# Performance work log

Hardware: AMD Instinct MI355X
Metric: run time of the kernel (lower is better)

## Reference

```python
import jax, jax.numpy as jnp
import numpy as np

B, L, C, H = 4, 2048, 512, 8
CH = C // H
EPS = 1e-5


def setup_inputs() -> dict:
    key = jax.random.key(0)
    k1, k2, k3 = jax.random.split(key, 3)
    return {
        "input_x": jax.random.normal(k1, (B, L, C), dtype=jnp.float32),
        "gamma": jnp.ones((C,), dtype=jnp.float32),
        "beta": jnp.zeros((C,), dtype=jnp.float32),
        "w_xyz": jax.random.normal(k2, (C, 3 * C), dtype=jnp.float32) * 0.02,
        "b_xyz": jnp.zeros((3 * C,), dtype=jnp.float32),
        "w_end": jax.random.normal(k3, (C, C), dtype=jnp.float32) * 0.02,
        "b_end": jnp.zeros((C,), dtype=jnp.float32),
    }


def reference(input_x, gamma, beta, w_xyz, b_xyz, w_end, b_end):
    b, l, c = input_x.shape
    h = H
    ch = c // h
    scale = 1.0 / np.sqrt(ch).astype(np.float32)

    # LayerNorm
    mu = jnp.mean(input_x, axis=-1, keepdims=True)
    var = jnp.var(input_x, axis=-1, keepdims=True)
    xn = (input_x - mu) / jnp.sqrt(var + EPS) * gamma + beta

    # xyz projection -> (3, b, h, l, ch)
    xyz = (xn @ w_xyz + b_xyz).reshape(b, l, 3, h, ch).transpose(2, 0, 3, 1, 4)
    q, k, v = xyz[0], xyz[1], xyz[2]

    # dot-product relevancy with sqr scale
    scores = jnp.einsum("bhqc,bhkc->bhqk", q * scale, k)
    attn = jax.nn.softmax(scores, axis=-1)

    # weighted sum -> (b, l, c)
    z = jnp.einsum("bhqk,bhkc->bhqc", attn, v).transpose(0, 2, 1, 3).reshape(b, l, c)
    z = z @ w_end + b_end
    return input_x + z
```

## Files before the change

### kernel.cpp

```cpp
#include <hip/hip_runtime.h>
#include <hip/hip_bf16.h>
#include <math.h>

constexpr int Bv = 4, Lv = 2048, Cv = 512, Hv = 8, CHv = 64;
constexpr int Mv = Bv * Lv;
constexpr int N3 = 3 * Cv;
constexpr float EPSv = 1e-5f;
constexpr float SCALEv = 0.125f;
constexpr float K2v = 0.125f * 1.44269504089f;
constexpr int LDST = 76;
constexpr int PSTR = 68;

typedef __attribute__((ext_vector_type(4))) float f32x4;
typedef __attribute__((ext_vector_type(8))) short bf16x8;

__device__ inline unsigned short f2bf(float f) {
  unsigned int u = __float_as_uint(f);
  unsigned int r = (u + 0x7fffu + ((u >> 16) & 1u)) >> 16;
  return (unsigned short)r;
}

__device__ __forceinline__ void async_copy16(void* lp, const void* gp) {
  __builtin_amdgcn_global_load_lds(
      (const __attribute__((address_space(1))) void*)gp,
      (__attribute__((address_space(3))) void*)lp, 16, 0, 0);
}

__global__ __launch_bounds__(256) void ln_kernel(const float* __restrict__ x,
                                                 const float* __restrict__ gamma,
                                                 const float* __restrict__ beta,
                                                 unsigned short* __restrict__ xnb) {
  const int row = blockIdx.x * 4 + (threadIdx.x >> 6);
  const int lane = threadIdx.x & 63;
  const float4* xr = reinterpret_cast<const float4*>(x + (size_t)row * Cv);
  float4 v0 = xr[lane];
  float4 v1 = xr[lane + 64];
  float s = v0.x + v0.y + v0.z + v0.w + v1.x + v1.y + v1.z + v1.w;
  float q = v0.x * v0.x + v0.y * v0.y + v0.z * v0.z + v0.w * v0.w +
            v1.x * v1.x + v1.y * v1.y + v1.z * v1.z + v1.w * v1.w;
#pragma unroll
  for (int m = 1; m < 64; m <<= 1) {
    s += __shfl_xor(s, m, 64);
    q += __shfl_xor(q, m, 64);
  }
  const float mu = s * (1.0f / Cv);
  const float var = q * (1.0f / Cv) - mu * mu;
  const float rstd = rsqrtf(var + EPSv);
  const float4* g4 = reinterpret_cast<const float4*>(gamma);
  const float4* b4 = reinterpret_cast<const float4*>(beta);
  float4 ga = g4[lane], gb = g4[lane + 64];
  float4 ba = b4[lane], bb = b4[lane + 64];
  ushort4 u0, u1;
  u0.x = f2bf((v0.x - mu) * rstd * ga.x + ba.x);
  u0.y = f2bf((v0.y - mu) * rstd * ga.y + ba.y);
  u0.z = f2bf((v0.z - mu) * rstd * ga.z + ba.z);
  u0.w = f2bf((v0.w - mu) * rstd * ga.w + ba.w);
  u1.x = f2bf((v1.x - mu) * rstd * gb.x + bb.x);
  u1.y = f2bf((v1.y - mu) * rstd * gb.y + bb.y);
  u1.z = f2bf((v1.z - mu) * rstd * gb.z + bb.z);
  u1.w = f2bf((v1.w - mu) * rstd * gb.w + bb.w);
  ushort4* xo = reinterpret_cast<ushort4*>(xnb + (size_t)row * Cv);
  xo[lane] = u0;
  xo[lane + 64] = u1;
}

__global__ __launch_bounds__(256) void transpose_f2b(const float* __restrict__ in,
                                                     unsigned short* __restrict__ out,
                                                     int R, int Cn) {
  __shared__ float Tl[64][65];
  const int t = threadIdx.x;
  const int tr = t >> 6, tc = t & 63;
  const int r0 = blockIdx.y * 64, c0 = blockIdx.x * 64;
#pragma unroll
  for (int i = 0; i < 16; ++i)
    Tl[tr + i * 4][tc] = in[(size_t)(r0 + tr + i * 4) * Cn + c0 + tc];
  __syncthreads();
#pragma unroll
  for (int i = 0; i < 16; ++i)
    out[(size_t)(c0 + tr + i * 4) * R + r0 + tc] = f2bf(Tl[tc][tr + i * 4]);
}

template <bool RES, bool OUTBF>
__global__ __launch_bounds__(256) void gemm_mfma(const unsigned short* __restrict__ A,
                                                 const unsigned short* __restrict__ Bt,
                                                 const float* __restrict__ bias,
                                                 const float* __restrict__ res,
                                                 float* __restrict__ Cf,
                                                 unsigned short* __restrict__ Cb,
                                                 int M, int N, int K) {
  __shared__ unsigned short Al[128 * 64];
  __shared__ unsigned short Bl[128 * 64];
  const int t = threadIdx.x;
  const int l = t & 63, w = t >> 6;
  const int lm = l & 15, lq = l >> 4;
  const int m0 = blockIdx.y * 128, n0 = blockIdx.x * 128;
  const int rw0 = (w >> 1) * 64, cw0 = (w & 1) * 64;

  f32x4 acc[4][4];
#pragma unroll
  for (int mi = 0; mi < 4; ++mi)
#pragma unroll
    for (int ni = 0; ni < 4; ++ni) acc[mi][ni] = f32x4{0.f, 0.f, 0.f, 0.f};

  const int sr8 = l >> 3;
  const int sc = l & 7;

  for (int k0 = 0; k0 < K; k0 += 64) {
#pragma unroll
    for (int j = 0; j < 4; ++j) {
      const int row = w * 32 + j * 8 + sr8;
      const int cs = sc ^ (row & 7);
      async_copy16(&Al[(w * 32 + j * 8) * 64],
                   A + (size_t)(m0 + row) * K + k0 + cs * 8);
      async_copy16(&Bl[(w * 32 + j * 8) * 64],
                   Bt + (size_t)(n0 + row) * K + k0 + cs * 8);
    }
    __syncthreads();

    bf16x8 af[4][2], bfr[4][2];
#pragma unroll
    for (int mi = 0; mi < 4; ++mi) {
      const int r = rw0 + mi * 16 + lm;
#pragma unroll
      for (int ks = 0; ks < 2; ++ks) {
        const int c = (ks * 4 + lq) ^ (r & 7);
        af[mi][ks] = *reinterpret_cast<const bf16x8*>(&Al[r * 64 + c * 8]);
      }
    }
#pragma unroll
    for (int ni = 0; ni < 4; ++ni) {
      const int r = cw0 + ni * 16 + lm;
#pragma unroll
      for (int ks = 0; ks < 2; ++ks) {
        const int c = (ks * 4 + lq) ^ (r & 7);
        bfr[ni][ks] = *reinterpret_cast<const bf16x8*>(&Bl[r * 64 + c * 8]);
      }
    }
#pragma unroll
    for (int ks = 0; ks < 2; ++ks)
#pragma unroll
      for (int mi = 0; mi < 4; ++mi)
#pragma unroll
        for (int ni = 0; ni < 4; ++ni)
          acc[mi][ni] = __builtin_amdgcn_mfma_f32_16x16x32_bf16(
              af[mi][ks], bfr[ni][ks], acc[mi][ni], 0, 0, 0);
    __syncthreads();
  }

#pragma unroll
  for (int mi = 0; mi < 4; ++mi)
#pragma unroll
    for (int ni = 0; ni < 4; ++ni) {
      const int col = n0 + cw0 + ni * 16 + lm;
      const float bv = bias[col];
#pragma unroll
      for (int r = 0; r < 4; ++r) {
        const int row = m0 + rw0 + mi * 16 + lq * 4 + r;
        float v = acc[mi][ni][r] + bv;
        if (RES) v += res[(size_t)row * N + col];
        if (OUTBF)
          Cb[(size_t)row * N + col] = f2bf(v);
        else
          Cf[(size_t)row * N + col] = v;
      }
    }
}

__global__ __launch_bounds__(256) void attn_mfma(const unsigned short* __restrict__ qkv,
                                                 unsigned short* __restrict__ zb) {
  __shared__ unsigned short Ks[64 * LDST];
  __shared__ unsigned short Vt[64 * LDST];
  __shared__ unsigned short Ps[64 * PSTR];

  const int t = threadIdx.x;
  const int l = t & 63, w = t >> 6;
  const int lm = l & 15, lq = l >> 4;

  const int f = blockIdx.x + 32 * blockIdx.y + 256 * blockIdx.z;
  const int n = (f & 7) * 128 + (f >> 3);
  const int qt = n & 31, h = (n >> 5) & 7, b = n >> 8;
  const int q0 = qt * 64;

  const unsigned short* base = qkv + (size_t)b * Lv * N3;
  const int kcol = Cv + h * CHv, vcol = 2 * Cv + h * CHv;

  bf16x8 qf0, qf1;
  {
    const unsigned short* qp = base + (size_t)(q0 + w * 16 + lm) * N3 + h * CHv + lq * 8;
    qf0 = *reinterpret_cast<const bf16x8*>(qp);
    qf1 = *reinterpret_cast<const bf16x8*>(qp + 32);
  }

  const int sr = t >> 3, sc = t & 7;

  bf16x8 kr0, kr1, vr0, vr1;
  {
    const unsigned short* kp = base + (size_t)sr * N3 + kcol + sc * 8;
    const unsigned short* vp = base + (size_t)sr * N3 + vcol + sc * 8;
    kr0 = *reinterpret_cast<const bf16x8*>(kp);
    kr1 = *reinterpret_cast<const bf16x8*>(kp + (size_t)32 * N3);
    vr0 = *reinterpret_cast<const bf16x8*>(vp);
    vr1 = *reinterpret_cast<const bf16x8*>(vp + (size_t)32 * N3);
  }

  f32x4 accO[4];
#pragma unroll
  for (int i = 0; i < 4; ++i) accO[i] = f32x4{0.f, 0.f, 0.f, 0.f};
  float m2 = -INFINITY;
  float lsum = 0.f;

  for (int kt = 0; kt < Lv / 64; ++kt) {
    __syncthreads();
    *reinterpret_cast<bf16x8*>(&Ks[sr * LDST + sc * 8]) = kr0;
    *reinterpret_cast<bf16x8*>(&Ks[(sr + 32) * LDST + sc * 8]) = kr1;
    {
      const unsigned short* v0 = reinterpret_cast<const unsigned short*>(&vr0);
      const unsigned short* v1 = reinterpret_cast<const unsigned short*>(&vr1);
#pragma unroll
      for (int j = 0; j < 8; ++j) {
        Vt[(sc * 8 + j) * LDST + (sr ^ (sc << 3))] = v0[j];
        Vt[(sc * 8 + j) * LDST + ((sr + 32) ^ (sc << 3))] = v1[j];
      }
    }
    __syncthreads();

    if (kt + 1 < Lv / 64) {
      const unsigned short* kp = base + (size_t)((kt + 1) * 64 + sr) * N3 + kcol + sc * 8;
      const unsigned short* vp = base + (size_t)((kt + 1) * 64 + sr) * N3 + vcol + sc * 8;
      kr0 = *reinterpret_cast<const bf16x8*>(kp);
      kr1 = *reinterpret_cast<const bf16x8*>(kp + (size_t)32 * N3);
      vr0 = *reinterpret_cast<const bf16x8*>(vp);
      vr1 = *reinterpret_cast<const bf16x8*>(vp + (size_t)32 * N3);
    }

    f32x4 sacc[4];
#pragma unroll
    for (int s = 0; s < 4; ++s) {
      bf16x8 kf0 = *reinterpret_cast<const bf16x8*>(&Ks[(16 * s + lm) * LDST + lq * 8]);
      bf16x8 kf1 = *reinterpret_cast<const bf16x8*>(&Ks[(16 * s + lm) * LDST + lq * 8 + 32]);
      f32x4 zz = f32x4{0.f, 0.f, 0.f, 0.f};
      sacc[s] = __builtin_amdgcn_mfma_f32_16x16x32_bf16(kf0, qf0, zz, 0, 0, 0);
      sacc[s] = __builtin_amdgcn_mfma_f32_16x16x32_bf16(kf1, qf1, sacc[s], 0, 0, 0);
    }

    f32x4 m4 = __builtin_elementwise_max(__builtin_elementwise_max(sacc[0], sacc[1]),
                                         __builtin_elementwise_max(sacc[2], sacc[3]));
    float mx = fmaxf(fmaxf(m4[0], m4[1]), fmaxf(m4[2], m4[3]));
    mx = fmaxf(mx, __shfl_xor(mx, 16));
    mx = fmaxf(mx, __shfl_xor(mx, 32));
    const float m2new = fmaxf(m2, mx * K2v);

    f32x4 ps[4];
#pragma unroll
    for (int s = 0; s < 4; ++s)
#pragma unroll
      for (int r = 0; r < 4; ++r)
        ps[s][r] = exp2f(sacc[s][r] * K2v - m2new);

#pragma unroll
    for (int s = 0; s < 4; ++s) {
      uint2 pk;
      pk.x = (unsigned)f2bf(ps[s][0]) | ((unsigned)f2bf(ps[s][1]) << 16);
      pk.y = (unsigned)f2bf(ps[s][2]) | ((unsigned)f2bf(ps[s][3]) << 16);
      *reinterpret_cast<uint2*>(&Ps[(w * 16 + lm) * PSTR + 16 * s + 4 * lq]) = pk;
    }

    f32x4 s4 = (ps[0] + ps[1]) + (ps[2] + ps[3]);
    float psum = (s4[0] + s4[1]) + (s4[2] + s4[3]);
    psum += __shfl_xor(psum, 16);
    psum += __shfl_xor(psum, 32);

    const float cf = exp2f(m2 - m2new);
    lsum = lsum * cf + psum;
    m2 = m2new;
#pragma unroll
    for (int r = 0; r < 4; ++r) {
      const float cfr = __shfl(cf, lq * 4 + r);
      accO[0][r] *= cfr;
      accO[1][r] *= cfr;
      accO[2][r] *= cfr;
      accO[3][r] *= cfr;
    }

#pragma unroll
    for (int ks = 0; ks < 2; ++ks) {
      bf16x8 pf = *reinterpret_cast<const bf16x8*>(&Ps[(w * 16 + lm) * PSTR + ks * 32 + lq * 8]);
#pragma unroll
      for (int ot = 0; ot < 4; ++ot) {
        const int ch = 16 * ot + lm;
        const int x = ch >> 3;
        bf16x8 vf = *reinterpret_cast<const bf16x8*>(&Vt[ch * LDST + (((4 * ks + lq) ^ x) << 3)]);
        accO[ot] = __builtin_amdgcn_mfma_f32_16x16x32_bf16(pf, vf, accO[ot], 0, 0, 0);
      }
    }
  }

#pragma unroll
  for (int r = 0; r < 4; ++r) {
    const float inv = 1.0f / __shfl(lsum, lq * 4 + r);
    const size_t row = (size_t)(b * Lv + q0 + w * 16 + lq * 4 + r);
#pragma unroll
    for (int ot = 0; ot < 4; ++ot)
      zb[row * Cv + h * CHv + 16 * ot + lm] = f2bf(accO[ot][r] * inv);
  }
}

extern "C" void kernel_launch(void* const* d_in, const int* in_sizes, int n_in,
                              void* d_out, int out_size, void* d_ws, size_t ws_size,
                              hipStream_t stream) {
  const float* x = (const float*)d_in[0];
  const float* gamma = (const float*)d_in[1];
  const float* beta = (const float*)d_in[2];
  const float* w_xyz = (const float*)d_in[3];
  const float* b_xyz = (const float*)d_in[4];
  const float* w_end = (const float*)d_in[5];
  const float* b_end = (const float*)d_in[6];
  float* out = (float*)d_out;

  unsigned short* xnb = (unsigned short*)d_ws;
  unsigned short* qkvb = xnb + (size_t)Mv * Cv;
  unsigned short* zb = qkvb + (size_t)Mv * N3;
  unsigned short* wxT = zb + (size_t)Mv * Cv;
  unsigned short* weT = wxT + (size_t)N3 * Cv;

  transpose_f2b<<<dim3(N3 / 64, Cv / 64), 256, 0, stream>>>(w_xyz, wxT, Cv, N3);
  transpose_f2b<<<dim3(Cv / 64, Cv / 64), 256, 0, stream>>>(w_end, weT, Cv, Cv);
  ln_kernel<<<Mv / 4, 256, 0, stream>>>(x, gamma, beta, xnb);
  gemm_mfma<false, true><<<dim3(N3 / 128, Mv / 128), 256, 0, stream>>>(
      xnb, wxT, b_xyz, nullptr, nullptr, qkvb, Mv, N3, Cv);
  attn_mfma<<<dim3(Lv / 64, Hv, Bv), 256, 0, stream>>>(qkvb, zb);
  gemm_mfma<true, false><<<dim3(Cv / 128, Mv / 128), 256, 0, stream>>>(
      zb, weT, b_end, x, out, nullptr, Mv, Cv, Cv);
}
```

Measured before the change: 225.0 us.

## Pre-transpose V in QKV GEMM and double-buffer attention tiles with async LDS loads

The QKV GEMM epilogue now writes V directly in a per-head transposed layout, so attention no longer scatters V into LDS element by element. The attention kernel uses 512-thread blocks covering 128 queries, double-buffers K/V tiles through async global-to-LDS copies with XOR swizzle, and drops one barrier per iteration. It also skips the softmax rescale unless the running max grows by more than a threshold. This trades an extra workspace buffer and larger LDS use per block for less shuffle and sync overhead.

```diff
diff --git a/kernel.cpp b/kernel.cpp
--- a/kernel.cpp
+++ b/kernel.cpp
@@ -6,10 +6,8 @@
 constexpr int Mv = Bv * Lv;
 constexpr int N3 = 3 * Cv;
 constexpr float EPSv = 1e-5f;
-constexpr float SCALEv = 0.125f;
 constexpr float K2v = 0.125f * 1.44269504089f;
-constexpr int LDST = 76;
-constexpr int PSTR = 68;
+constexpr int PSTR = 72;
 
 typedef __attribute__((ext_vector_type(4))) float f32x4;
 typedef __attribute__((ext_vector_type(8))) short bf16x8;
@@ -80,13 +78,14 @@
     out[(size_t)(c0 + tr + i * 4) * R + r0 + tc] = f2bf(Tl[tc][tr + i * 4]);
 }
 
-template <bool RES, bool OUTBF>
+template <bool RES, bool OUTBF, bool VOUT>
 __global__ __launch_bounds__(256) void gemm_mfma(const unsigned short* __restrict__ A,
                                                  const unsigned short* __restrict__ Bt,
                                                  const float* __restrict__ bias,
                                                  const float* __restrict__ res,
                                                  float* __restrict__ Cf,
                                                  unsigned short* __restrict__ Cb,
+                                                 unsigned short* __restrict__ vTp,
                                                  int M, int N, int K) {
   __shared__ unsigned short Al[128 * 64];
   __shared__ unsigned short Bl[128 * 64];
@@ -153,36 +152,52 @@
     for (int ni = 0; ni < 4; ++ni) {
       const int col = n0 + cw0 + ni * 16 + lm;
       const float bv = bias[col];
-#pragma unroll
-      for (int r = 0; r < 4; ++r) {
-        const int row = m0 + rw0 + mi * 16 + lq * 4 + r;
-        float v = acc[mi][ni][r] + bv;
-        if (RES) v += res[(size_t)row * N + col];
-        if (OUTBF)
-          Cb[(size_t)row * N + col] = f2bf(v);
-        else
-          Cf[(size_t)row * N + col] = v;
-      }
-    }
-}
-
-__global__ __launch_bounds__(256) void attn_mfma(const unsigned short* __restrict__ qkv,
+      if (VOUT && col >= 1024) {
+        const int cc = col - 1024;
+        const int hh = cc >> 6, chh = cc & 63;
+        const int row0 = m0 + rw0 + mi * 16 + lq * 4;
+        const int bb = row0 >> 11, l0 = row0 & 2047;
+        ushort4 u;
+        u.x = f2bf(acc[mi][ni][0] + bv);
+        u.y = f2bf(acc[mi][ni][1] + bv);
+        u.z = f2bf(acc[mi][ni][2] + bv);
+        u.w = f2bf(acc[mi][ni][3] + bv);
+        *reinterpret_cast<ushort4*>(
+            &vTp[(((size_t)bb * 8 + hh) * 64 + chh) * 2048 + l0]) = u;
+      } else {
+#pragma unroll
+        for (int r = 0; r < 4; ++r) {
+          const int row = m0 + rw0 + mi * 16 + lq * 4 + r;
+          float v = acc[mi][ni][r] + bv;
+          if (RES) v += res[(size_t)row * N + col];
+          if (OUTBF)
+            Cb[(size_t)row * N + col] = f2bf(v);
+          else
+            Cf[(size_t)row * N + col] = v;
+        }
+      }
+    }
+}
+
+__global__ __launch_bounds__(512) void attn_mfma(const unsigned short* __restrict__ qkv,
+                                                 const unsigned short* __restrict__ vT,
                                                  unsigned short* __restrict__ zb) {
-  __shared__ unsigned short Ks[64 * LDST];
-  __shared__ unsigned short Vt[64 * LDST];
-  __shared__ unsigned short Ps[64 * PSTR];
+  __shared__ unsigned short Ks[2][64 * 64];
+  __shared__ unsigned short Vt[2][64 * 64];
+  __shared__ unsigned short Ps[128 * PSTR];
 
   const int t = threadIdx.x;
   const int l = t & 63, w = t >> 6;
   const int lm = l & 15, lq = l >> 4;
 
-  const int f = blockIdx.x + 32 * blockIdx.y + 256 * blockIdx.z;
-  const int n = (f & 7) * 128 + (f >> 3);
-  const int qt = n & 31, h = (n >> 5) & 7, b = n >> 8;
-  const int q0 = qt * 64;
+  const int f = blockIdx.x;
+  const int n = (f & 7) * 64 + (f >> 3);
+  const int qt = n & 15, h = (n >> 4) & 7, b = n >> 7;
+  const int q0 = qt * 128;
 
   const unsigned short* base = qkv + (size_t)b * Lv * N3;
-  const int kcol = Cv + h * CHv, vcol = 2 * Cv + h * CHv;
+  const unsigned short* vbase = vT + ((size_t)b * 8 + h) * 64 * 2048;
+  const int kcol = Cv + h * CHv;
 
   bf16x8 qf0, qf1;
   {
@@ -191,17 +206,9 @@
     qf1 = *reinterpret_cast<const bf16x8*>(qp + 32);
   }
 
-  const int sr = t >> 3, sc = t & 7;
-
-  bf16x8 kr0, kr1, vr0, vr1;
-  {
-    const unsigned short* kp = base + (size_t)sr * N3 + kcol + sc * 8;
-    const unsigned short* vp = base + (size_t)sr * N3 + vcol + sc * 8;
-    kr0 = *reinterpret_cast<const bf16x8*>(kp);
-    kr1 = *reinterpret_cast<const bf16x8*>(kp + (size_t)32 * N3);
-    vr0 = *reinterpret_cast<const bf16x8*>(vp);
-    vr1 = *reinterpret_cast<const bf16x8*>(vp + (size_t)32 * N3);
-  }
+  const int sr8 = l >> 3;
+  const int scs = (l & 7) ^ sr8;
+  const int krow = w * 8 + sr8;
 
   f32x4 accO[4];
 #pragma unroll
@@ -209,35 +216,29 @@
   float m2 = -INFINITY;
   float lsum = 0.f;
 
+  async_copy16(&Ks[0][w * 8 * 64], base + (size_t)krow * N3 + kcol + scs * 8);
+  async_copy16(&Vt[0][w * 8 * 64], vbase + (size_t)krow * 2048 + 0 + scs * 8);
+
   for (int kt = 0; kt < Lv / 64; ++kt) {
     __syncthreads();
-    *reinterpret_cast<bf16x8*>(&Ks[sr * LDST + sc * 8]) = kr0;
-    *reinterpret_cast<bf16x8*>(&Ks[(sr + 32) * LDST + sc * 8]) = kr1;
-    {
-      const unsigned short* v0 = reinterpret_cast<const unsigned short*>(&vr0);
-      const unsigned short* v1 = reinterpret_cast<const unsigned short*>(&vr1);
-#pragma unroll
-      for (int j = 0; j < 8; ++j) {
-        Vt[(sc * 8 + j) * LDST + (sr ^ (sc << 3))] = v0[j];
-        Vt[(sc * 8 + j) * LDST + ((sr + 32) ^ (sc << 3))] = v1[j];
-      }
-    }
-    __syncthreads();
 
     if (kt + 1 < Lv / 64) {
-      const unsigned short* kp = base + (size_t)((kt + 1) * 64 + sr) * N3 + kcol + sc * 8;
-      const unsigned short* vp = base + (size_t)((kt + 1) * 64 + sr) * N3 + vcol + sc * 8;
-      kr0 = *reinterpret_cast<const bf16x8*>(kp);
-      kr1 = *reinterpret_cast<const bf16x8*>(kp + (size_t)32 * N3);
-      vr0 = *reinterpret_cast<const bf16x8*>(vp);
-      vr1 = *reinterpret_cast<const bf16x8*>(vp + (size_t)32 * N3);
-    }
+      const int nb = (kt + 1) & 1;
+      async_copy16(&Ks[nb][w * 8 * 64],
+                   base + (size_t)((kt + 1) * 64 + krow) * N3 + kcol + scs * 8);
+      async_copy16(&Vt[nb][w * 8 * 64],
+                   vbase + (size_t)krow * 2048 + (kt + 1) * 64 + scs * 8);
+    }
+
+    const unsigned short* Kb = &Ks[kt & 1][0];
+    const unsigned short* Vb = &Vt[kt & 1][0];
 
     f32x4 sacc[4];
 #pragma unroll
     for (int s = 0; s < 4; ++s) {
-      bf16x8 kf0 = *reinterpret_cast<const bf16x8*>(&Ks[(16 * s + lm) * LDST + lq * 8]);
-      bf16x8 kf1 = *reinterpret_cast<const bf16x8*>(&Ks[(16 * s + lm) * LDST + lq * 8 + 32]);
+      const int r = 16 * s + lm;
+      bf16x8 kf0 = *reinterpret_cast<const bf16x8*>(&Kb[r * 64 + (lq ^ (lm & 7)) * 8]);
+      bf16x8 kf1 = *reinterpret_cast<const bf16x8*>(&Kb[r * 64 + ((4 + lq) ^ (lm & 7)) * 8]);
       f32x4 zz = f32x4{0.f, 0.f, 0.f, 0.f};
       sacc[s] = __builtin_amdgcn_mfma_f32_16x16x32_bf16(kf0, qf0, zz, 0, 0, 0);
       sacc[s] = __builtin_amdgcn_mfma_f32_16x16x32_bf16(kf1, qf1, sacc[s], 0, 0, 0);
@@ -248,14 +249,28 @@
     float mx = fmaxf(fmaxf(m4[0], m4[1]), fmaxf(m4[2], m4[3]));
     mx = fmaxf(mx, __shfl_xor(mx, 16));
     mx = fmaxf(mx, __shfl_xor(mx, 32));
-    const float m2new = fmaxf(m2, mx * K2v);
+    const float mxs = mx * K2v;
+    if (!__all(mxs - m2 <= 8.0f)) {
+      const float m2n = fmaxf(m2, mxs);
+      const float cf = exp2f(m2 - m2n);
+      lsum *= cf;
+      m2 = m2n;
+#pragma unroll
+      for (int r = 0; r < 4; ++r) {
+        const float cfr = __shfl(cf, lq * 4 + r);
+        accO[0][r] *= cfr;
+        accO[1][r] *= cfr;
+        accO[2][r] *= cfr;
+        accO[3][r] *= cfr;
+      }
+    }
 
     f32x4 ps[4];
 #pragma unroll
     for (int s = 0; s < 4; ++s)
 #pragma unroll
       for (int r = 0; r < 4; ++r)
-        ps[s][r] = exp2f(sacc[s][r] * K2v - m2new);
+        ps[s][r] = exp2f(sacc[s][r] * K2v - m2);
 
 #pragma unroll
     for (int s = 0; s < 4; ++s) {
@@ -269,18 +284,7 @@
     float psum = (s4[0] + s4[1]) + (s4[2] + s4[3]);
     psum += __shfl_xor(psum, 16);
     psum += __shfl_xor(psum, 32);
-
-    const float cf = exp2f(m2 - m2new);
-    lsum = lsum * cf + psum;
-    m2 = m2new;
-#pragma unroll
-    for (int r = 0; r < 4; ++r) {
-      const float cfr = __shfl(cf, lq * 4 + r);
-      accO[0][r] *= cfr;
-      accO[1][r] *= cfr;
-      accO[2][r] *= cfr;
-      accO[3][r] *= cfr;
-    }
+    lsum += psum;
 
 #pragma unroll
     for (int ks = 0; ks < 2; ++ks) {
@@ -288,8 +292,8 @@
 #pragma unroll
       for (int ot = 0; ot < 4; ++ot) {
         const int ch = 16 * ot + lm;
-        const int x = ch >> 3;
-        bf16x8 vf = *reinterpret_cast<const bf16x8*>(&Vt[ch * LDST + (((4 * ks + lq) ^ x) << 3)]);
+        bf16x8 vf = *reinterpret_cast<const bf16x8*>(
+            &Vb[ch * 64 + ((4 * ks + lq) ^ (lm & 7)) * 8]);
         accO[ot] = __builtin_amdgcn_mfma_f32_16x16x32_bf16(pf, vf, accO[ot], 0, 0, 0);
       }
     }
@@ -322,13 +326,14 @@
   unsigned short* zb = qkvb + (size_t)Mv * N3;
   unsigned short* wxT = zb + (size_t)Mv * Cv;
   unsigned short* weT = wxT + (size_t)N3 * Cv;
+  unsigned short* vTb = weT + (size_t)Cv * Cv;
 
   transpose_f2b<<<dim3(N3 / 64, Cv / 64), 256, 0, stream>>>(w_xyz, wxT, Cv, N3);
   transpose_f2b<<<dim3(Cv / 64, Cv / 64), 256, 0, stream>>>(w_end, weT, Cv, Cv);
   ln_kernel<<<Mv / 4, 256, 0, stream>>>(x, gamma, beta, xnb);
-  gemm_mfma<false, true><<<dim3(N3 / 128, Mv / 128), 256, 0, stream>>>(
-      xnb, wxT, b_xyz, nullptr, nullptr, qkvb, Mv, N3, Cv);
-  attn_mfma<<<dim3(Lv / 64, Hv, Bv), 256, 0, stream>>>(qkvb, zb);
-  gemm_mfma<true, false><<<dim3(Cv / 128, Mv / 128), 256, 0, stream>>>(
-      zb, weT, b_end, x, out, nullptr, Mv, Cv, Cv);
-}
+  gemm_mfma<false, true, true><<<dim3(N3 / 128, Mv / 128), 256, 0, stream>>>(
+      xnb, wxT, b_xyz, nullptr, nullptr, qkvb, vTb, Mv, N3, Cv);
+  attn_mfma<<<512, 512, 0, stream>>>(qkvb, vTb, zb);
+  gemm_mfma<true, false, false><<<dim3(Cv / 128, Mv / 128), 256, 0, stream>>>(
+      zb, weT, b_end, x, out, nullptr, nullptr, Mv, Cv, Cv);
+}
```

Result: faster. 205.9 us (-8.5%).
